# Kernel tuning notes

Measured on AMD Instinct MI355X. Metric: run time of the kernel, lower is better.

The kernel has to match this reference:

```python
import jax, jax.numpy as jnp
import numpy as np


def _weighted_combine(emb, w):
    # emb: [B, L, D], w: [B, L] -> [B, D]
    sw = jnp.sum(w, axis=1, keepdims=True)          # [B, 1]
    wn = (w / sw)[..., None]                         # [B, L, 1]
    return jnp.sum(emb * wn, axis=1)


def setup_inputs() -> dict:
    key = jax.random.key(0)
    k1, k2, k3, k4, k5, k6 = jax.random.split(key, 6)
    B, La, Lb, V, D = 16384, 50, 20, 100000, 64
    return {
        "ids_single": jax.random.randint(k1, (B,), 0, V, dtype=jnp.int32),
        "ids_multi_a": jax.random.randint(k2, (B, La), 0, V, dtype=jnp.int32),
        "ids_multi_b": jax.random.randint(k3, (B, Lb), 0, V, dtype=jnp.int32),
        "weights_a": jax.random.uniform(k4, (B, La), dtype=jnp.float32),
        "weights_b": jax.random.uniform(k5, (B, Lb), dtype=jnp.float32),
        "embedding_table": jax.random.normal(k6, (V, D), dtype=jnp.float32),
    }


def reference(ids_single, ids_multi_a, ids_multi_b, weights_a, weights_b, embedding_table):
    # Per-field gather (equivalent to the flat gather + split in the original)
    e_single = embedding_table[ids_single]        # [B, D]
    e_a = embedding_table[ids_multi_a]            # [B, La, D]
    e_b = embedding_table[ids_multi_b]            # [B, Lb, D]
    # 'weight' combiner: normalize weights per row and sum-pool
    p_a = _weighted_combine(e_a, weights_a)       # [B, D]
    p_b = _weighted_combine(e_b, weights_b)       # [B, D]
    # concat along feature dim (do_concat=True)
    return jnp.concatenate([e_single, p_a, p_b], axis=-1)  # [B, 3*D]
```

## Files before the change

### kernel.cpp

```cpp
#include <hip/hip_runtime.h>

#define BATCH 16384
#define LA 50
#define LB 20
#define DIM 64
#define NT_A 13
#define NT_B 5

__device__ __forceinline__ float4 ld4(const float* p) { return *(const float4*)p; }

__global__ __launch_bounds__(256) void emb_pool_kernel(
    const int*   __restrict__ ids_single,
    const int*   __restrict__ ids_a,
    const int*   __restrict__ ids_b,
    const float* __restrict__ wa,
    const float* __restrict__ wb,
    const float* __restrict__ table,
    float*       __restrict__ out)
{
    const int lane = (int)(threadIdx.x & 63);
    const int wave = (int)(threadIdx.x >> 6);
    const int q    = lane >> 4;
    const int j    = lane & 15;
    const int b    = (int)blockIdx.x * 4 + wave;

    const char* tbl = (const char*)table;
    const uint32_t jb = (uint32_t)(j << 4);

    const int*   ia  = ids_a + (size_t)b * LA;
    const float* wpa = wa    + (size_t)b * LA;
    const int*   ib  = ids_b + (size_t)b * LB;
    const float* wpb = wb    + (size_t)b * LB;

    const int   aid = ia[lane < LA ? lane : LA - 1];
    const float aw  = (lane < LA) ? wpa[lane] : 0.0f;
    const int   bid = ib[lane < LB ? lane : LB - 1];
    const float bw  = (lane < LB) ? wpb[lane] : 0.0f;
    const int   sid = ids_single[b];

    float swa = aw, swb = bw;
#pragma unroll
    for (int m = 1; m < 64; m <<= 1) {
        swa += __shfl_xor(swa, m);
        swb += __shfl_xor(swb, m);
    }
    const float inva = 1.0f / swa;
    const float invb = 1.0f / swb;

    uint32_t offA[NT_A]; float wA[NT_A];
#pragma unroll
    for (int t = 0; t < NT_A; ++t) {
        const int src = 4 * t + q;
        offA[t] = ((uint32_t)__shfl(aid, src) << 8) + jb;
        wA[t]   = __shfl(aw, src);
    }
    uint32_t offB[NT_B]; float wB[NT_B];
#pragma unroll
    for (int t = 0; t < NT_B; ++t) {
        const int src = 4 * t + q;
        offB[t] = ((uint32_t)__shfl(bid, src) << 8) + jb;
        wB[t]   = __shfl(bw, src);
    }
    const uint32_t offS = ((uint32_t)sid << 8) + jb;

    float4 rA[NT_A];
#pragma unroll
    for (int t = 0; t < NT_A; ++t) rA[t] = ld4((const float*)(tbl + offA[t]));
    float4 rB[NT_B];
#pragma unroll
    for (int t = 0; t < NT_B; ++t) rB[t] = ld4((const float*)(tbl + offB[t]));
    const float4 rS = ld4((const float*)(tbl + offS));

    float4 accA = make_float4(0.f, 0.f, 0.f, 0.f);
#pragma unroll
    for (int t = 0; t < NT_A; ++t) {
        accA.x += wA[t] * rA[t].x; accA.y += wA[t] * rA[t].y;
        accA.z += wA[t] * rA[t].z; accA.w += wA[t] * rA[t].w;
    }
    float4 accB = make_float4(0.f, 0.f, 0.f, 0.f);
#pragma unroll
    for (int t = 0; t < NT_B; ++t) {
        accB.x += wB[t] * rB[t].x; accB.y += wB[t] * rB[t].y;
        accB.z += wB[t] * rB[t].z; accB.w += wB[t] * rB[t].w;
    }

#pragma unroll
    for (int m = 16; m <= 32; m <<= 1) {
        accA.x += __shfl_xor(accA.x, m); accA.y += __shfl_xor(accA.y, m);
        accA.z += __shfl_xor(accA.z, m); accA.w += __shfl_xor(accA.w, m);
        accB.x += __shfl_xor(accB.x, m); accB.y += __shfl_xor(accB.y, m);
        accB.z += __shfl_xor(accB.z, m); accB.w += __shfl_xor(accB.w, m);
    }

    if (q == 0) {
        float* orow = out + (size_t)b * (3 * DIM);
        *(float4*)(orow + j * 4) = rS;
        float4 oa; oa.x = accA.x * inva; oa.y = accA.y * inva;
                   oa.z = accA.z * inva; oa.w = accA.w * inva;
        *(float4*)(orow + DIM + j * 4) = oa;
        float4 ob; ob.x = accB.x * invb; ob.y = accB.y * invb;
                   ob.z = accB.z * invb; ob.w = accB.w * invb;
        *(float4*)(orow + 2 * DIM + j * 4) = ob;
    }
}

extern "C" void kernel_launch(void* const* d_in, const int* in_sizes, int n_in,
                              void* d_out, int out_size, void* d_ws, size_t ws_size,
                              hipStream_t stream) {
    const int*   ids_single = (const int*)  d_in[0];
    const int*   ids_a      = (const int*)  d_in[1];
    const int*   ids_b      = (const int*)  d_in[2];
    const float* wa         = (const float*)d_in[3];
    const float* wb         = (const float*)d_in[4];
    const float* table      = (const float*)d_in[5];
    float*       out        = (float*)d_out;

    emb_pool_kernel<<<BATCH / 4, 256, 0, stream>>>(ids_single, ids_a, ids_b,
                                                   wa, wb, table, out);
}
```

Before: 119.2 us.

## Convert embedding table to bf16 in workspace before the gather-pool kernel

A pre-pass kernel converts the fp32 embedding table to bf16 with round-to-nearest-even into the workspace on every call. The pooling kernel then gathers 128-byte bf16 rows instead of 256-byte fp32 rows and widens them to fp32 for accumulation. The aim is to halve the bytes moved by the random gathers, which dominate cost. In exchange it adds a full-table conversion pass each call and introduces bf16 rounding error, including on the directly copied single-id embedding.

```diff
diff --git a/kernel.cpp b/kernel.cpp
--- a/kernel.cpp
+++ b/kernel.cpp
@@ -6,17 +6,33 @@
 #define DIM 64
 #define NT_A 13
 #define NT_B 5
+#define VOCAB 100000
 
-__device__ __forceinline__ float4 ld4(const float* p) { return *(const float4*)p; }
+__global__ __launch_bounds__(256) void tbl_to_bf16_kernel(
+    const uint4* __restrict__ src, uint2* __restrict__ dst)
+{
+    const int i = (int)blockIdx.x * 256 + (int)threadIdx.x;
+    uint4 v = src[i];
+    auto cvt = [](uint32_t x) -> uint32_t {
+        return (x + 0x7fffu + ((x >> 16) & 1u)) >> 16;
+    };
+    uint2 o;
+    o.x = cvt(v.x) | (cvt(v.y) << 16);
+    o.y = cvt(v.z) | (cvt(v.w) << 16);
+    dst[i] = o;
+}
+
+__device__ __forceinline__ float bflo(uint32_t d) { return __uint_as_float(d << 16); }
+__device__ __forceinline__ float bfhi(uint32_t d) { return __uint_as_float(d & 0xFFFF0000u); }
 
 __global__ __launch_bounds__(256) void emb_pool_kernel(
-    const int*   __restrict__ ids_single,
-    const int*   __restrict__ ids_a,
-    const int*   __restrict__ ids_b,
-    const float* __restrict__ wa,
-    const float* __restrict__ wb,
-    const float* __restrict__ table,
-    float*       __restrict__ out)
+    const int*    __restrict__ ids_single,
+    const int*    __restrict__ ids_a,
+    const int*    __restrict__ ids_b,
+    const float*  __restrict__ wa,
+    const float*  __restrict__ wb,
+    const ushort* __restrict__ tbl16,
+    float*        __restrict__ out)
 {
     const int lane = (int)(threadIdx.x & 63);
     const int wave = (int)(threadIdx.x >> 6);
@@ -24,8 +40,8 @@
     const int j    = lane & 15;
     const int b    = (int)blockIdx.x * 4 + wave;
 
-    const char* tbl = (const char*)table;
-    const uint32_t jb = (uint32_t)(j << 4);
+    const char* tbl = (const char*)tbl16;
+    const uint32_t jb = (uint32_t)(j << 3);
 
     const int*   ia  = ids_a + (size_t)b * LA;
     const float* wpa = wa    + (size_t)b * LA;
@@ -51,37 +67,40 @@
 #pragma unroll
     for (int t = 0; t < NT_A; ++t) {
         const int src = 4 * t + q;
-        offA[t] = ((uint32_t)__shfl(aid, src) << 8) + jb;
+        offA[t] = ((uint32_t)__shfl(aid, src) << 7) + jb;
         wA[t]   = __shfl(aw, src);
     }
     uint32_t offB[NT_B]; float wB[NT_B];
 #pragma unroll
     for (int t = 0; t < NT_B; ++t) {
         const int src = 4 * t + q;
-        offB[t] = ((uint32_t)__shfl(bid, src) << 8) + jb;
+        offB[t] = ((uint32_t)__shfl(bid, src) << 7) + jb;
         wB[t]   = __shfl(bw, src);
     }
-    const uint32_t offS = ((uint32_t)sid << 8) + jb;
 
-    float4 rA[NT_A];
+    uint2 rA[NT_A];
 #pragma unroll
-    for (int t = 0; t < NT_A; ++t) rA[t] = ld4((const float*)(tbl + offA[t]));
-    float4 rB[NT_B];
+    for (int t = 0; t < NT_A; ++t) rA[t] = *(const uint2*)(tbl + offA[t]);
+    uint2 rB[NT_B];
 #pragma unroll
-    for (int t = 0; t < NT_B; ++t) rB[t] = ld4((const float*)(tbl + offB[t]));
-    const float4 rS = ld4((const float*)(tbl + offS));
+    for (int t = 0; t < NT_B; ++t) rB[t] = *(const uint2*)(tbl + offB[t]);
+    uint2 rS = make_uint2(0u, 0u);
+    if (q == 0)
+        rS = *(const uint2*)(tbl + (((uint32_t)sid << 7) + jb));
 
     float4 accA = make_float4(0.f, 0.f, 0.f, 0.f);
 #pragma unroll
     for (int t = 0; t < NT_A; ++t) {
-        accA.x += wA[t] * rA[t].x; accA.y += wA[t] * rA[t].y;
-        accA.z += wA[t] * rA[t].z; accA.w += wA[t] * rA[t].w;
+        const float w = wA[t];
+        accA.x += w * bflo(rA[t].x); accA.y += w * bfhi(rA[t].x);
+        accA.z += w * bflo(rA[t].y); accA.w += w * bfhi(rA[t].y);
     }
     float4 accB = make_float4(0.f, 0.f, 0.f, 0.f);
 #pragma unroll
     for (int t = 0; t < NT_B; ++t) {
-        accB.x += wB[t] * rB[t].x; accB.y += wB[t] * rB[t].y;
-        accB.z += wB[t] * rB[t].z; accB.w += wB[t] * rB[t].w;
+        const float w = wB[t];
+        accB.x += w * bflo(rB[t].x); accB.y += w * bfhi(rB[t].x);
+        accB.z += w * bflo(rB[t].y); accB.w += w * bfhi(rB[t].y);
     }
 
 #pragma unroll
@@ -94,12 +113,17 @@
 
     if (q == 0) {
         float* orow = out + (size_t)b * (3 * DIM);
-        *(float4*)(orow + j * 4) = rS;
-        float4 oa; oa.x = accA.x * inva; oa.y = accA.y * inva;
-                   oa.z = accA.z * inva; oa.w = accA.w * inva;
+        float4 os;
+        os.x = bflo(rS.x); os.y = bfhi(rS.x);
+        os.z = bflo(rS.y); os.w = bfhi(rS.y);
+        *(float4*)(orow + j * 4) = os;
+        float4 oa;
+        oa.x = accA.x * inva; oa.y = accA.y * inva;
+        oa.z = accA.z * inva; oa.w = accA.w * inva;
         *(float4*)(orow + DIM + j * 4) = oa;
-        float4 ob; ob.x = accB.x * invb; ob.y = accB.y * invb;
-                   ob.z = accB.z * invb; ob.w = accB.w * invb;
+        float4 ob;
+        ob.x = accB.x * invb; ob.y = accB.y * invb;
+        ob.z = accB.z * invb; ob.w = accB.w * invb;
         *(float4*)(orow + 2 * DIM + j * 4) = ob;
     }
 }
@@ -115,6 +139,11 @@
     const float* table      = (const float*)d_in[5];
     float*       out        = (float*)d_out;
 
+    const int n4 = VOCAB * DIM / 4;
+    tbl_to_bf16_kernel<<<n4 / 256, 256, 0, stream>>>((const uint4*)table,
+                                                     (uint2*)d_ws);
+
     emb_pool_kernel<<<BATCH / 4, 256, 0, stream>>>(ids_single, ids_a, ids_b,
-                                                   wa, wb, table, out);
+                                                   wa, wb,
+                                                   (const ushort*)d_ws, out);
 }
```

After: 107.1 us. 1.11x faster.
